# Optimization experiments

Hardware: AMD Instinct MI355X
Metric: run time of the kernel (lower is better)

Reference implementation:

```python
import jax, jax.numpy as jnp
import numpy as np

EMB_DIM = 1024
NUM_HEADS = 16
HEAD_DIM = EMB_DIM // NUM_HEADS
B, S = 4, 2048


def setup_inputs() -> dict:
    key = jax.random.key(0)
    ks = jax.random.split(key, 16)
    def lin(k):
        return jax.random.normal(k, (EMB_DIM, EMB_DIM), jnp.float32) * (EMB_DIM ** -0.5)
    x = jax.random.normal(ks[0], (B, S, EMB_DIM), jnp.float32)
    positions = jnp.sort(jax.random.randint(ks[1], (B, S), 0, 100000), axis=-1)
    return {
        "x": x,
        "positions": positions,
        "Wq": lin(ks[2]), "bq": jnp.zeros((EMB_DIM,), jnp.float32),
        "Wk": lin(ks[3]), "bk": jnp.zeros((EMB_DIM,), jnp.float32),
        "Wv": lin(ks[4]), "bv": jnp.zeros((EMB_DIM,), jnp.float32),
        "Wo": lin(ks[5]), "bo": jnp.zeros((EMB_DIM,), jnp.float32),
        "q_scale": jnp.ones((EMB_DIM,), jnp.float32),
        "k_scale": jnp.ones((EMB_DIM,), jnp.float32),
        "v_scale": jnp.ones((EMB_DIM,), jnp.float32),
        "o_scale": jnp.ones((EMB_DIM,), jnp.float32),
    }


def _rotate(t, cos, sin):
    # t: (B, H, S, D); pairs of consecutive dims rotated by per-position angles.
    # cos/sin: (B, 1, S, D/2)
    tp = t.reshape(t.shape[:-1] + (HEAD_DIM // 2, 2))
    t0, t1 = tp[..., 0], tp[..., 1]
    r0 = t0 * cos - t1 * sin
    r1 = t0 * sin + t1 * cos
    return jnp.stack([r0, r1], axis=-1).reshape(t.shape)


def reference(x, positions, Wq, bq, Wk, bk, Wv, bv, Wo, bo,
              q_scale, k_scale, v_scale, o_scale):
    b, s, e = x.shape
    # theta_vector: standard RoPE inverse frequencies for head_dim
    theta = 1.0 / (10000.0 ** (jnp.arange(0, HEAD_DIM, 2, dtype=jnp.float32) / HEAD_DIM))
    angles = positions.astype(jnp.float32)[..., None] * theta  # (B, S, D/2)
    cos = jnp.cos(angles)[:, None, :, :]  # (B, 1, S, D/2)
    sin = jnp.sin(angles)[:, None, :, :]

    def proj(W, bias, scale):
        y = (x @ W + bias) * scale
        return y.reshape(b, s, NUM_HEADS, HEAD_DIM).transpose(0, 2, 1, 3)  # (B,H,S,D)

    Q = _rotate(proj(Wq, bq, q_scale), cos, sin)
    K = _rotate(proj(Wk, bk, k_scale), cos, sin)
    V = proj(Wv, bv, v_scale)

    scores = jnp.einsum('bhqd,bhkd->bhqk', Q, K) / jnp.sqrt(
        jnp.asarray(HEAD_DIM, jnp.float32))
    probs = jax.nn.softmax(scores, axis=-1)
    context = jnp.einsum('bhqk,bhkd->bhqd', probs, V)
    context = context.transpose(0, 2, 1, 3).reshape(b, s, e)
    return (context @ Wo + bo) * o_scale
```

## Files before the change

### kernel.cpp

```cpp
#include <hip/hip_runtime.h>
#include <hip/hip_bf16.h>

using bf16 = __hip_bfloat16;
typedef __attribute__((ext_vector_type(8))) short short8;
typedef __attribute__((ext_vector_type(4))) float f32x4;
typedef __attribute__((ext_vector_type(16))) float f32x16;

#define AS1 __attribute__((address_space(1)))
#define AS3 __attribute__((address_space(3)))

__device__ __forceinline__ void gload_lds16(const void* g, void* l) {
  __builtin_amdgcn_global_load_lds((const AS1 unsigned int*)g,
                                   (AS3 unsigned int*)l, 16, 0, 0);
}

__device__ __forceinline__ unsigned cvtpk_bf16(float lo, float hi) {
  unsigned r;
  asm("v_cvt_pk_bf16_f32 %0, %1, %2" : "=v"(r) : "v"(lo), "v"(hi));
  return r;
}

__device__ __forceinline__ void pl32swap(unsigned &a, unsigned &b) {
  asm("v_permlane32_swap_b32 %0, %1" : "+v"(a), "+v"(b));
}

__global__ __launch_bounds__(256) void k_convert(const float* __restrict__ src,
                                                 bf16* __restrict__ dst, int n4) {
  int i = blockIdx.x * 256 + threadIdx.x;
  if (i >= n4) return;
  float4 v = reinterpret_cast<const float4*>(src)[i];
  alignas(8) bf16 o[4] = {__float2bfloat16(v.x), __float2bfloat16(v.y),
                          __float2bfloat16(v.z), __float2bfloat16(v.w)};
  *reinterpret_cast<uint2*>(dst + (size_t)i * 4) = *reinterpret_cast<uint2*>(o);
}

__global__ __launch_bounds__(256) void k_wtrans(
    const float* __restrict__ W0, const float* __restrict__ W1,
    const float* __restrict__ W2, const float* __restrict__ W3,
    bf16* __restrict__ T0, bf16* __restrict__ T1,
    bf16* __restrict__ T2, bf16* __restrict__ T3) {
  __shared__ float tile[64][65];
  const float* W; bf16* T;
  switch (blockIdx.z) {
    case 0: W = W0; T = T0; break;
    case 1: W = W1; T = T1; break;
    case 2: W = W2; T = T2; break;
    default: W = W3; T = T3; break;
  }
  const int k0 = blockIdx.x * 64, n0 = blockIdx.y * 64;
  const int r = threadIdx.x >> 6, c = threadIdx.x & 63;
#pragma unroll
  for (int i = 0; i < 16; i++)
    tile[r + i * 4][c] = W[(size_t)(k0 + r + i * 4) * 1024 + n0 + c];
  __syncthreads();
#pragma unroll
  for (int i = 0; i < 16; i++)
    T[(size_t)(n0 + r + i * 4) * 1024 + k0 + c] = __float2bfloat16(tile[c][r + i * 4]);
}

template <int OUT_F32>
__global__ __launch_bounds__(256) void k_gemm_bt(
    const bf16* __restrict__ A, const bf16* __restrict__ BT,
    const float* __restrict__ bias, const float* __restrict__ scale,
    void* __restrict__ Cout, int M, int N, int K) {
  __shared__ alignas(16) bf16 sA[128 * 32];
  __shared__ alignas(16) bf16 sB[128 * 32];
  const int lane = threadIdx.x & 63;
  const int wid = threadIdx.x >> 6;
  const int wr = wid >> 1, wc = wid & 1;
  const int m0 = blockIdx.x * 128;
  const int n0 = blockIdx.y * 128;

  f32x4 acc[4][4];
#pragma unroll
  for (int i = 0; i < 4; i++)
#pragma unroll
    for (int j = 0; j < 4; j++) acc[i][j] = f32x4{0.f, 0.f, 0.f, 0.f};

  const int srow = lane >> 2;
  const int scol = (lane & 3) * 8;

  for (int k0 = 0; k0 < K; k0 += 32) {
    __syncthreads();
#pragma unroll
    for (int cc = 0; cc < 2; cc++) {
      const int chunk = wid + cc * 4;
      gload_lds16(A + (size_t)(m0 + chunk * 16 + srow) * K + k0 + scol,
                  sA + chunk * 512);
      gload_lds16(BT + (size_t)(n0 + chunk * 16 + srow) * K + k0 + scol,
                  sB + chunk * 512);
    }
    __syncthreads();
    short8 af[4], bfr[4];
#pragma unroll
    for (int i = 0; i < 4; i++) {
      af[i] = *reinterpret_cast<const short8*>(
          sA + (wr * 64 + i * 16 + (lane & 15)) * 32 + (lane >> 4) * 8);
      bfr[i] = *reinterpret_cast<const short8*>(
          sB + (wc * 64 + i * 16 + (lane & 15)) * 32 + (lane >> 4) * 8);
    }
#pragma unroll
    for (int mi = 0; mi < 4; mi++)
#pragma unroll
      for (int ni = 0; ni < 4; ni++)
        acc[mi][ni] = __builtin_amdgcn_mfma_f32_16x16x32_bf16(
            af[mi], bfr[ni], acc[mi][ni], 0, 0, 0);
  }

#pragma unroll
  for (int ni = 0; ni < 4; ni++) {
    const int n = n0 + wc * 64 + ni * 16 + (lane & 15);
    const float bz = bias[n];
    const float sc = scale[n];
#pragma unroll
    for (int mi = 0; mi < 4; mi++) {
      const int mr = m0 + wr * 64 + mi * 16 + (lane >> 4) * 4;
#pragma unroll
      for (int j = 0; j < 4; j++) {
        float v = (acc[mi][ni][j] + bz) * sc;
        if (OUT_F32)
          reinterpret_cast<float*>(Cout)[(size_t)(mr + j) * N + n] = v;
        else
          reinterpret_cast<bf16*>(Cout)[(size_t)(mr + j) * N + n] = __float2bfloat16(v);
      }
    }
  }
}

__global__ __launch_bounds__(256) void k_rope(const bf16* __restrict__ Y,
                                              const int* __restrict__ pos,
                                              bf16* __restrict__ Out, float mul) {
  const int idx = blockIdx.x * 256 + threadIdx.x;
  const int i = idx & 31;
  const int h = (idx >> 5) & 15;
  const int s = (idx >> 9) & 2047;
  const int b = idx >> 20;
  const float p = (float)pos[b * 2048 + s];
  const float ex = (float)(2 * i) * (1.0f / 64.0f);
  const float theta = 1.0f / powf(10000.0f, ex);
  const float ang = p * theta;
  float sn, cs;
  sincosf(ang, &sn, &cs);
  const size_t ybase = ((size_t)(b * 2048 + s)) * 1024 + h * 64 + 2 * i;
  ushort2 tv = *reinterpret_cast<const ushort2*>(Y + ybase);
  const float f0 = __uint_as_float(((unsigned)tv.x) << 16);
  const float f1 = __uint_as_float(((unsigned)tv.y) << 16);
  const float r0 = (f0 * cs - f1 * sn) * mul;
  const float r1 = (f0 * sn + f1 * cs) * mul;
  alignas(4) bf16 o2[2] = {__float2bfloat16(r0), __float2bfloat16(r1)};
  const size_t obase = (((size_t)(b * 16 + h)) * 2048 + s) * 64 + 2 * i;
  *reinterpret_cast<ushort2*>(Out + obase) = *reinterpret_cast<ushort2*>(o2);
}

__global__ __launch_bounds__(256) void k_vtrans(const bf16* __restrict__ Yv,
                                                bf16* __restrict__ VT) {
  __shared__ bf16 tile[64][66];
  const int s0 = blockIdx.x * 64;
  const int bh = blockIdx.y;
  const int b = bh >> 4, h = bh & 15;
  const int r = threadIdx.x >> 6, c = threadIdx.x & 63;
#pragma unroll
  for (int i = 0; i < 16; i++)
    tile[r + i * 4][c] = Yv[(size_t)(b * 2048 + s0 + r + i * 4) * 1024 + h * 64 + c];
  __syncthreads();
#pragma unroll
  for (int i = 0; i < 16; i++)
    VT[((size_t)bh * 64 + r + i * 4) * 2048 + s0 + c] = tile[c][r + i * 4];
}

__global__ __launch_bounds__(256, 2) void k_attn(const bf16* __restrict__ Q,
                                                 const bf16* __restrict__ Kt,
                                                 const bf16* __restrict__ VT,
                                                 bf16* __restrict__ Ctx) {
  __shared__ alignas(16) bf16 sK[2][64 * 64];
  __shared__ alignas(16) bf16 sV[2][64 * 64];

  const int lane = threadIdx.x & 63;
  const int w = threadIdx.x >> 6;
  const int q0 = blockIdx.x * 128;
  const int bh = blockIdx.y;
  const int b = bh >> 4, h = bh & 15;
  const int ql = lane & 31;
  const int hi = lane >> 5;
  const int r8 = lane >> 3;
  const int gslot = (lane & 7) ^ r8;

  const bf16* Qrow = Q + ((size_t)bh * 2048 + q0 + w * 32 + ql) * 64;
  short8 qf[4];
#pragma unroll
  for (int ks = 0; ks < 4; ks++)
    qf[ks] = *reinterpret_cast<const short8*>(Qrow + ks * 16 + hi * 8);

  f32x16 accO[2];
#pragma unroll
  for (int dt = 0; dt < 2; dt++)
#pragma unroll
    for (int r = 0; r < 16; r++) accO[dt][r] = 0.f;
  float m = -1e30f, l = 0.f;

  const size_t kbase = (size_t)bh * 2048 * 64;
  const size_t vbase = (size_t)bh * 64 * 2048;

#pragma unroll
  for (int cc = 0; cc < 2; cc++) {
    const int ch = w + cc * 4, row = ch * 8 + r8;
    gload_lds16(Kt + kbase + (size_t)row * 64 + gslot * 8, &sK[0][ch * 512]);
    gload_lds16(VT + vbase + (size_t)row * 2048 + gslot * 8, &sV[0][ch * 512]);
  }

  for (int it = 0; it < 32; ++it) {
    __syncthreads();
    const int cur = it & 1;
    if (it + 1 < 32) {
      const int nxt = cur ^ 1, kt = (it + 1) * 64;
#pragma unroll
      for (int cc = 0; cc < 2; cc++) {
        const int ch = w + cc * 4, row = ch * 8 + r8;
        gload_lds16(Kt + kbase + (size_t)(kt + row) * 64 + gslot * 8,
                    &sK[nxt][ch * 512]);
        gload_lds16(VT + vbase + (size_t)row * 2048 + kt + gslot * 8,
                    &sV[nxt][ch * 512]);
      }
    }

    f32x16 accS[2];
#pragma unroll
    for (int t = 0; t < 2; t++) {
#pragma unroll
      for (int r = 0; r < 16; r++) accS[t][r] = 0.f;
#pragma unroll
      for (int ks = 0; ks < 4; ks++) {
        const int row = 32 * t + ql;
        const int cs = (2 * ks + hi) ^ (lane & 7);
        short8 kf = *reinterpret_cast<const short8*>(&sK[cur][row * 64 + cs * 8]);
        accS[t] =
            __builtin_amdgcn_mfma_f32_32x32x16_bf16(kf, qf[ks], accS[t], 0, 0, 0);
      }
    }

    float pmax = -1e30f;
#pragma unroll
    for (int t = 0; t < 2; t++)
#pragma unroll
      for (int r = 0; r < 16; r++) pmax = fmaxf(pmax, accS[t][r]);
    pmax = fmaxf(pmax, __shfl_xor(pmax, 32, 64));
    if (__any(pmax - m > 11.0f)) {
      const float mn = fmaxf(m, pmax);
      const float al = exp2f(m - mn);
      m = mn;
      l *= al;
#pragma unroll
      for (int dt = 0; dt < 2; dt++)
#pragma unroll
        for (int r = 0; r < 16; r++) accO[dt][r] *= al;
    }
    float s = 0.f;
#pragma unroll
    for (int t = 0; t < 2; t++)
#pragma unroll
      for (int r = 0; r < 16; r++) {
        const float p = exp2f(accS[t][r] - m);
        accS[t][r] = p;
        s += p;
      }
    s += __shfl_xor(s, 32, 64);
    l += s;

#pragma unroll
    for (int ss = 0; ss < 4; ss++) {
      const int t = ss >> 1, base = (ss & 1) * 8;
      unsigned w01 = cvtpk_bf16(accS[t][base + 0], accS[t][base + 1]);
      unsigned w23 = cvtpk_bf16(accS[t][base + 2], accS[t][base + 3]);
      unsigned w45 = cvtpk_bf16(accS[t][base + 4], accS[t][base + 5]);
      unsigned w67 = cvtpk_bf16(accS[t][base + 6], accS[t][base + 7]);
      pl32swap(w01, w45);
      pl32swap(w23, w67);
      uint4 pau = {w01, w23, w45, w67};
      short8 pa = *reinterpret_cast<short8*>(&pau);
#pragma unroll
      for (int dt = 0; dt < 2; dt++) {
        const int row = 32 * dt + ql;
        const int cs = (2 * ss + hi) ^ (lane & 7);
        short8 vf = *reinterpret_cast<const short8*>(&sV[cur][row * 64 + cs * 8]);
        accO[dt] =
            __builtin_amdgcn_mfma_f32_32x32x16_bf16(vf, pa, accO[dt], 0, 0, 0);
      }
    }
  }

  __syncthreads();
  bf16* tw = &sK[0][0] + w * 2048;
  const float inv = 1.0f / l;
#pragma unroll
  for (int dt = 0; dt < 2; dt++)
#pragma unroll
    for (int g = 0; g < 4; g++) {
      unsigned wa = cvtpk_bf16(accO[dt][4 * g + 0] * inv, accO[dt][4 * g + 1] * inv);
      unsigned wb = cvtpk_bf16(accO[dt][4 * g + 2] * inv, accO[dt][4 * g + 3] * inv);
      const int c = (4 * dt + g) ^ (ql & 7);
      uint2 val = {wa, wb};
      *reinterpret_cast<uint2*>(tw + ql * 64 + c * 8 + hi * 4) = val;
    }
  __syncthreads();
  const int qr = lane >> 1, half = lane & 1;
  const size_t orow = (((size_t)b * 2048 + q0 + w * 32 + qr) * 16 + h) * 64;
#pragma unroll
  for (int i = 0; i < 4; i++) {
    const int c2 = (half * 4 + i) ^ (qr & 7);
    short8 v = *reinterpret_cast<const short8*>(tw + qr * 64 + c2 * 8);
    *reinterpret_cast<short8*>(Ctx + orow + half * 32 + i * 8) = v;
  }
}

extern "C" void kernel_launch(void* const* d_in, const int* in_sizes, int n_in,
                              void* d_out, int out_size, void* d_ws, size_t ws_size,
                              hipStream_t stream) {
  const float* x = (const float*)d_in[0];
  const int* positions = (const int*)d_in[1];
  const float* Wq = (const float*)d_in[2];
  const float* bq = (const float*)d_in[3];
  const float* Wk = (const float*)d_in[4];
  const float* bk = (const float*)d_in[5];
  const float* Wv = (const float*)d_in[6];
  const float* bv = (const float*)d_in[7];
  const float* Wo = (const float*)d_in[8];
  const float* bo = (const float*)d_in[9];
  const float* q_scale = (const float*)d_in[10];
  const float* k_scale = (const float*)d_in[11];
  const float* v_scale = (const float*)d_in[12];
  const float* o_scale = (const float*)d_in[13];
  float* out = (float*)d_out;

  char* ws = (char*)d_ws;
  bf16* xb  = (bf16*)(ws);
  bf16* WTq = (bf16*)(ws + (16u << 20));
  bf16* WTk = WTq + (1u << 20);
  bf16* WTv = WTk + (1u << 20);
  bf16* WTo = WTv + (1u << 20);
  bf16* Yq  = (bf16*)(ws + (24u << 20));
  bf16* Yk  = (bf16*)(ws + (40u << 20));
  bf16* Yv  = (bf16*)(ws + (56u << 20));
  bf16* Qr  = xb;
  bf16* Kr  = Yq;
  bf16* VT  = Yk;
  bf16* Ctx = Yv;

  const int M = 8192, N = 1024, K = 1024;

  k_convert<<<8192, 256, 0, stream>>>(x, xb, M * K / 4);
  k_wtrans<<<dim3(16, 16, 4), 256, 0, stream>>>(Wq, Wk, Wv, Wo, WTq, WTk, WTv, WTo);

  k_gemm_bt<0><<<dim3(64, 8), 256, 0, stream>>>(xb, WTq, bq, q_scale, Yq, M, N, K);
  k_gemm_bt<0><<<dim3(64, 8), 256, 0, stream>>>(xb, WTk, bk, k_scale, Yk, M, N, K);
  k_gemm_bt<0><<<dim3(64, 8), 256, 0, stream>>>(xb, WTv, bv, v_scale, Yv, M, N, K);

  k_rope<<<16384, 256, 0, stream>>>(Yq, positions, Qr, 0.18033688011112042f);
  k_rope<<<16384, 256, 0, stream>>>(Yk, positions, Kr, 1.0f);
  k_vtrans<<<dim3(32, 64), 256, 0, stream>>>(Yv, VT);

  k_attn<<<dim3(16, 64), 256, 0, stream>>>(Qr, Kr, VT, Ctx);

  k_gemm_bt<1><<<dim3(64, 8), 256, 0, stream>>>(Ctx, WTo, bo, o_scale, out, M, N, K);
}
```

Baseline: 399.5 us.

## Merge QKV GEMMs, vectorize RoPE, widen attention blocks to 512 threads

The three Q/K/V projection GEMMs become one launch with a 24-wide N grid that relies on WTq/WTk/WTv and Yq/Yk/Yv being contiguous in the workspace. RoPE now has each thread handle 16 elements with 16-byte loads and stores instead of 2 elements. The attention kernel uses 512-thread blocks covering 256 queries, so each K/V tile load into LDS is shared by 8 waves instead of 4, and the row max uses three-input max chains. These changes cut launch count and global-memory traffic per unit of work, but the larger attention blocks raise LDS and register pressure per block.

```diff
diff --git a/kernel.cpp b/kernel.cpp
--- a/kernel.cpp
+++ b/kernel.cpp
@@ -22,6 +22,10 @@
 
 __device__ __forceinline__ void pl32swap(unsigned &a, unsigned &b) {
   asm("v_permlane32_swap_b32 %0, %1" : "+v"(a), "+v"(b));
+}
+
+__device__ __forceinline__ float fm3(float a, float b, float c) {
+  return fmaxf(fmaxf(a, b), c);
 }
 
 __global__ __launch_bounds__(256) void k_convert(const float* __restrict__ src,
@@ -58,11 +62,81 @@
     T[(size_t)(n0 + r + i * 4) * 1024 + k0 + c] = __float2bfloat16(tile[c][r + i * 4]);
 }
 
-template <int OUT_F32>
+__global__ __launch_bounds__(256) void k_gemm_qkv(
+    const bf16* __restrict__ A, const bf16* __restrict__ BT,
+    const float* __restrict__ bq, const float* __restrict__ bk,
+    const float* __restrict__ bv, const float* __restrict__ sq,
+    const float* __restrict__ sk, const float* __restrict__ sv,
+    bf16* __restrict__ Yqkv) {
+  __shared__ alignas(16) bf16 sA[128 * 32];
+  __shared__ alignas(16) bf16 sB[128 * 32];
+  const int K = 1024;
+  const int lane = threadIdx.x & 63;
+  const int wid = threadIdx.x >> 6;
+  const int wr = wid >> 1, wc = wid & 1;
+  const int m0 = blockIdx.x * 128;
+  const int n0 = blockIdx.y * 128;
+
+  f32x4 acc[4][4];
+#pragma unroll
+  for (int i = 0; i < 4; i++)
+#pragma unroll
+    for (int j = 0; j < 4; j++) acc[i][j] = f32x4{0.f, 0.f, 0.f, 0.f};
+
+  const int srow = lane >> 2;
+  const int scol = (lane & 3) * 8;
+
+  for (int k0 = 0; k0 < K; k0 += 32) {
+    __syncthreads();
+#pragma unroll
+    for (int cc = 0; cc < 2; cc++) {
+      const int chunk = wid + cc * 4;
+      gload_lds16(A + (size_t)(m0 + chunk * 16 + srow) * K + k0 + scol,
+                  sA + chunk * 512);
+      gload_lds16(BT + (size_t)(n0 + chunk * 16 + srow) * K + k0 + scol,
+                  sB + chunk * 512);
+    }
+    __syncthreads();
+    short8 af[4], bfr[4];
+#pragma unroll
+    for (int i = 0; i < 4; i++) {
+      af[i] = *reinterpret_cast<const short8*>(
+          sA + (wr * 64 + i * 16 + (lane & 15)) * 32 + (lane >> 4) * 8);
+      bfr[i] = *reinterpret_cast<const short8*>(
+          sB + (wc * 64 + i * 16 + (lane & 15)) * 32 + (lane >> 4) * 8);
+    }
+#pragma unroll
+    for (int mi = 0; mi < 4; mi++)
+#pragma unroll
+      for (int ni = 0; ni < 4; ni++)
+        acc[mi][ni] = __builtin_amdgcn_mfma_f32_16x16x32_bf16(
+            af[mi], bfr[ni], acc[mi][ni], 0, 0, 0);
+  }
+
+  const int seg = n0 >> 10;
+  bf16* dst = Yqkv + (size_t)seg * (8u << 20);
+  const float* bias = seg == 0 ? bq : (seg == 1 ? bk : bv);
+  const float* scale = seg == 0 ? sq : (seg == 1 ? sk : sv);
+  const int nb = n0 & 1023;
+#pragma unroll
+  for (int ni = 0; ni < 4; ni++) {
+    const int n = nb + wc * 64 + ni * 16 + (lane & 15);
+    const float bz = bias[n];
+    const float sc = scale[n];
+#pragma unroll
+    for (int mi = 0; mi < 4; mi++) {
+      const int mr = m0 + wr * 64 + mi * 16 + (lane >> 4) * 4;
+#pragma unroll
+      for (int j = 0; j < 4; j++)
+        dst[(size_t)(mr + j) * 1024 + n] = __float2bfloat16((acc[mi][ni][j] + bz) * sc);
+    }
+  }
+}
+
 __global__ __launch_bounds__(256) void k_gemm_bt(
     const bf16* __restrict__ A, const bf16* __restrict__ BT,
     const float* __restrict__ bias, const float* __restrict__ scale,
-    void* __restrict__ Cout, int M, int N, int K) {
+    float* __restrict__ Cout, int M, int N, int K) {
   __shared__ alignas(16) bf16 sA[128 * 32];
   __shared__ alignas(16) bf16 sB[128 * 32];
   const int lane = threadIdx.x & 63;
@@ -116,13 +190,8 @@
     for (int mi = 0; mi < 4; mi++) {
       const int mr = m0 + wr * 64 + mi * 16 + (lane >> 4) * 4;
 #pragma unroll
-      for (int j = 0; j < 4; j++) {
-        float v = (acc[mi][ni][j] + bz) * sc;
-        if (OUT_F32)
-          reinterpret_cast<float*>(Cout)[(size_t)(mr + j) * N + n] = v;
-        else
-          reinterpret_cast<bf16*>(Cout)[(size_t)(mr + j) * N + n] = __float2bfloat16(v);
-      }
+      for (int j = 0; j < 4; j++)
+        Cout[(size_t)(mr + j) * N + n] = (acc[mi][ni][j] + bz) * sc;
     }
   }
 }
@@ -131,25 +200,31 @@
                                               const int* __restrict__ pos,
                                               bf16* __restrict__ Out, float mul) {
   const int idx = blockIdx.x * 256 + threadIdx.x;
-  const int i = idx & 31;
-  const int h = (idx >> 5) & 15;
-  const int s = (idx >> 9) & 2047;
-  const int b = idx >> 20;
+  const int c = idx & 3;
+  const int h = (idx >> 2) & 15;
+  const int s = (idx >> 6) & 2047;
+  const int b = idx >> 17;
   const float p = (float)pos[b * 2048 + s];
-  const float ex = (float)(2 * i) * (1.0f / 64.0f);
-  const float theta = 1.0f / powf(10000.0f, ex);
-  const float ang = p * theta;
-  float sn, cs;
-  sincosf(ang, &sn, &cs);
-  const size_t ybase = ((size_t)(b * 2048 + s)) * 1024 + h * 64 + 2 * i;
-  ushort2 tv = *reinterpret_cast<const ushort2*>(Y + ybase);
-  const float f0 = __uint_as_float(((unsigned)tv.x) << 16);
-  const float f1 = __uint_as_float(((unsigned)tv.y) << 16);
-  const float r0 = (f0 * cs - f1 * sn) * mul;
-  const float r1 = (f0 * sn + f1 * cs) * mul;
-  alignas(4) bf16 o2[2] = {__float2bfloat16(r0), __float2bfloat16(r1)};
-  const size_t obase = (((size_t)(b * 16 + h)) * 2048 + s) * 64 + 2 * i;
-  *reinterpret_cast<ushort2*>(Out + obase) = *reinterpret_cast<ushort2*>(o2);
+  const size_t ybase = ((size_t)(b * 2048 + s)) * 1024 + h * 64 + c * 16;
+  const size_t obase = (((size_t)(b * 16 + h)) * 2048 + s) * 64 + c * 16;
+
+  union { short8 v[2]; short a[16]; } in, out;
+  in.v[0] = *reinterpret_cast<const short8*>(Y + ybase);
+  in.v[1] = *reinterpret_cast<const short8*>(Y + ybase + 8);
+#pragma unroll
+  for (int j = 0; j < 8; j++) {
+    const int i = c * 8 + j;
+    const float ex = (float)(2 * i) * (1.0f / 64.0f);
+    const float theta = 1.0f / powf(10000.0f, ex);
+    float sn, cs;
+    sincosf(p * theta, &sn, &cs);
+    const float f0 = __uint_as_float(((unsigned)(unsigned short)in.a[2 * j]) << 16);
+    const float f1 = __uint_as_float(((unsigned)(unsigned short)in.a[2 * j + 1]) << 16);
+    out.a[2 * j] = (short)__bfloat16_as_ushort(__float2bfloat16((f0 * cs - f1 * sn) * mul));
+    out.a[2 * j + 1] = (short)__bfloat16_as_ushort(__float2bfloat16((f0 * sn + f1 * cs) * mul));
+  }
+  *reinterpret_cast<short8*>(Out + obase) = out.v[0];
+  *reinterpret_cast<short8*>(Out + obase + 8) = out.v[1];
 }
 
 __global__ __launch_bounds__(256) void k_vtrans(const bf16* __restrict__ Yv,
@@ -168,22 +243,22 @@
     VT[((size_t)bh * 64 + r + i * 4) * 2048 + s0 + c] = tile[c][r + i * 4];
 }
 
-__global__ __launch_bounds__(256, 2) void k_attn(const bf16* __restrict__ Q,
+__global__ __launch_bounds__(512, 4) void k_attn(const bf16* __restrict__ Q,
                                                  const bf16* __restrict__ Kt,
                                                  const bf16* __restrict__ VT,
                                                  bf16* __restrict__ Ctx) {
-  __shared__ alignas(16) bf16 sK[2][64 * 64];
-  __shared__ alignas(16) bf16 sV[2][64 * 64];
+  __shared__ alignas(16) bf16 smem[4][4096];
 
   const int lane = threadIdx.x & 63;
   const int w = threadIdx.x >> 6;
-  const int q0 = blockIdx.x * 128;
+  const int q0 = blockIdx.x * 256;
   const int bh = blockIdx.y;
   const int b = bh >> 4, h = bh & 15;
   const int ql = lane & 31;
   const int hi = lane >> 5;
   const int r8 = lane >> 3;
   const int gslot = (lane & 7) ^ r8;
+  const int row_st = w * 8 + r8;
 
   const bf16* Qrow = Q + ((size_t)bh * 2048 + q0 + w * 32 + ql) * 64;
   short8 qf[4];
@@ -201,26 +276,18 @@
   const size_t kbase = (size_t)bh * 2048 * 64;
   const size_t vbase = (size_t)bh * 64 * 2048;
 
-#pragma unroll
-  for (int cc = 0; cc < 2; cc++) {
-    const int ch = w + cc * 4, row = ch * 8 + r8;
-    gload_lds16(Kt + kbase + (size_t)row * 64 + gslot * 8, &sK[0][ch * 512]);
-    gload_lds16(VT + vbase + (size_t)row * 2048 + gslot * 8, &sV[0][ch * 512]);
-  }
+  gload_lds16(Kt + kbase + (size_t)row_st * 64 + gslot * 8, &smem[0][w * 512]);
+  gload_lds16(VT + vbase + (size_t)row_st * 2048 + gslot * 8, &smem[2][w * 512]);
 
   for (int it = 0; it < 32; ++it) {
     __syncthreads();
     const int cur = it & 1;
     if (it + 1 < 32) {
       const int nxt = cur ^ 1, kt = (it + 1) * 64;
-#pragma unroll
-      for (int cc = 0; cc < 2; cc++) {
-        const int ch = w + cc * 4, row = ch * 8 + r8;
-        gload_lds16(Kt + kbase + (size_t)(kt + row) * 64 + gslot * 8,
-                    &sK[nxt][ch * 512]);
-        gload_lds16(VT + vbase + (size_t)row * 2048 + kt + gslot * 8,
-                    &sV[nxt][ch * 512]);
-      }
+      gload_lds16(Kt + kbase + (size_t)(kt + row_st) * 64 + gslot * 8,
+                  &smem[nxt][w * 512]);
+      gload_lds16(VT + vbase + (size_t)row_st * 2048 + kt + gslot * 8,
+                  &smem[2 + nxt][w * 512]);
     }
 
     f32x16 accS[2];
@@ -232,17 +299,17 @@
       for (int ks = 0; ks < 4; ks++) {
         const int row = 32 * t + ql;
         const int cs = (2 * ks + hi) ^ (lane & 7);
-        short8 kf = *reinterpret_cast<const short8*>(&sK[cur][row * 64 + cs * 8]);
+        short8 kf = *reinterpret_cast<const short8*>(&smem[cur][row * 64 + cs * 8]);
         accS[t] =
             __builtin_amdgcn_mfma_f32_32x32x16_bf16(kf, qf[ks], accS[t], 0, 0, 0);
       }
     }
 
-    float pmax = -1e30f;
-#pragma unroll
-    for (int t = 0; t < 2; t++)
-#pragma unroll
-      for (int r = 0; r < 16; r++) pmax = fmaxf(pmax, accS[t][r]);
+    float pmax = fmaxf(accS[0][0], accS[0][1]);
+#pragma unroll
+    for (int r = 2; r < 16; r += 2) pmax = fm3(pmax, accS[0][r], accS[0][r + 1]);
+#pragma unroll
+    for (int r = 0; r < 16; r += 2) pmax = fm3(pmax, accS[1][r], accS[1][r + 1]);
     pmax = fmaxf(pmax, __shfl_xor(pmax, 32, 64));
     if (__any(pmax - m > 11.0f)) {
       const float mn = fmaxf(m, pmax);
@@ -281,7 +348,8 @@
       for (int dt = 0; dt < 2; dt++) {
         const int row = 32 * dt + ql;
         const int cs = (2 * ss + hi) ^ (lane & 7);
-        short8 vf = *reinterpret_cast<const short8*>(&sV[cur][row * 64 + cs * 8]);
+        short8 vf =
+            *reinterpret_cast<const short8*>(&smem[2 + cur][row * 64 + cs * 8]);
         accO[dt] =
             __builtin_amdgcn_mfma_f32_32x32x16_bf16(vf, pa, accO[dt], 0, 0, 0);
       }
@@ -289,7 +357,7 @@
   }
 
   __syncthreads();
-  bf16* tw = &sK[0][0] + w * 2048;
+  bf16* tw = &smem[0][0] + w * 2048;
   const float inv = 1.0f / l;
 #pragma unroll
   for (int dt = 0; dt < 2; dt++)
@@ -350,15 +418,14 @@
   k_convert<<<8192, 256, 0, stream>>>(x, xb, M * K / 4);
   k_wtrans<<<dim3(16, 16, 4), 256, 0, stream>>>(Wq, Wk, Wv, Wo, WTq, WTk, WTv, WTo);
 
-  k_gemm_bt<0><<<dim3(64, 8), 256, 0, stream>>>(xb, WTq, bq, q_scale, Yq, M, N, K);
-  k_gemm_bt<0><<<dim3(64, 8), 256, 0, stream>>>(xb, WTk, bk, k_scale, Yk, M, N, K);
-  k_gemm_bt<0><<<dim3(64, 8), 256, 0, stream>>>(xb, WTv, bv, v_scale, Yv, M, N, K);
-
-  k_rope<<<16384, 256, 0, stream>>>(Yq, positions, Qr, 0.18033688011112042f);
-  k_rope<<<16384, 256, 0, stream>>>(Yk, positions, Kr, 1.0f);
+  k_gemm_qkv<<<dim3(64, 24), 256, 0, stream>>>(xb, WTq, bq, bk, bv,
+                                               q_scale, k_scale, v_scale, Yq);
+
+  k_rope<<<2048, 256, 0, stream>>>(Yq, positions, Qr, 0.18033688011112042f);
+  k_rope<<<2048, 256, 0, stream>>>(Yk, positions, Kr, 1.0f);
   k_vtrans<<<dim3(32, 64), 256, 0, stream>>>(Yv, VT);
 
-  k_attn<<<dim3(16, 64), 256, 0, stream>>>(Qr, Kr, VT, Ctx);
-
-  k_gemm_bt<1><<<dim3(64, 8), 256, 0, stream>>>(Ctx, WTo, bo, o_scale, out, M, N, K);
-}
+  k_attn<<<dim3(8, 64), 512, 0, stream>>>(Qr, Kr, VT, Ctx);
+
+  k_gemm_bt<<<dim3(64, 8), 256, 0, stream>>>(Ctx, WTo, bo, o_scale, out, M, N, K);
+}
```

Measured after the change: 378.9 us. 1.05x faster.
